# Performance work log

Measured on AMD Instinct MI355X. Metric: run time of the kernel, lower is better.

## Reference

```python
import jax, jax.numpy as jnp
import numpy as np

N, DIN, DH, DOUT, E, K = 8192, 1024, 4096, 1024, 8, 2
AUX_EPS = 1e-10


def setup_inputs() -> dict:
    key = jax.random.key(0)
    kx, kgw, kgb, kw1, kb1, kw2, kb2 = jax.random.split(key, 7)
    def init(k, shape, fan_in):
        return (jax.random.normal(k, shape, jnp.float32) / np.sqrt(fan_in)).astype(jnp.float32)
    return {
        "x": jax.random.normal(kx, (N, DIN), jnp.float32),
        "gate_w": init(kgw, (DIN, E), DIN),
        "gate_b": jnp.zeros((E,), jnp.float32),
        "w1": init(kw1, (E, DIN, DH), DIN),
        "b1": jnp.zeros((E, DH), jnp.float32),
        "w2": init(kw2, (E, DH, DOUT), DH),
        "b2": jnp.zeros((E, DOUT), jnp.float32),
    }


def reference(x, gate_w, gate_b, w1, b1, w2, b2):
    # Gating
    logits = x @ gate_w + gate_b                      # [N, E]
    probs = jax.nn.softmax(logits, axis=-1)           # [N, E]
    topk_vals, topk_idx = jax.lax.top_k(probs, K)     # [N, K]
    topk_norm = topk_vals / (topk_vals.sum(-1, keepdims=True) + AUX_EPS)

    # Scatter normalized top-k weights into a dense [N, E] combine matrix.
    n = x.shape[0]
    weights = jnp.zeros((n, E), x.dtype).at[jnp.arange(n)[:, None], topk_idx].add(topk_norm)

    # Dense all-expert FFN (same math: non-selected experts get weight 0).
    h = jax.nn.relu(jnp.einsum('nd,edh->neh', x, w1) + b1)   # [N, E, DH]
    y = jnp.einsum('neh,eho->neo', h, w2) + b2               # [N, E, DOUT]
    output = jnp.einsum('neo,ne->no', y, weights)            # [N, DOUT]

    # Aux load-balancing loss: KL(mean_probs || uniform)
    mean_probs = probs.mean(axis=0)
    aux_loss = jnp.sum(mean_probs * jnp.log(mean_probs * E + AUX_EPS))

    return output, aux_loss, probs
```

## Files before the change

### kernel.cpp

```cpp
#include <hip/hip_runtime.h>

#define NTOK 8192
#define DIN 1024
#define DH   4096
#define DOUT 1024
#define NE   8
#define MAXTILES 136
#define SLOTCAP  (MAXTILES*128)

typedef __bf16 bf16x8 __attribute__((ext_vector_type(8)));
typedef float  f32x4  __attribute__((ext_vector_type(4)));

constexpr size_t OFF_W1T  = 0;
constexpr size_t OFF_W2T  = 67108864;
constexpr size_t OFF_XB   = 134217728;
constexpr size_t OFF_H    = 150994944;
constexpr size_t OFF_SROW = 293601280;
constexpr size_t OFF_SW   = 293670912;
constexpr size_t OFF_TIDX = 293740544;
constexpr size_t OFF_TW   = 293806080;
constexpr size_t OFF_CTRL = 293871616;
constexpr size_t OFF_PART = 293871744;

__device__ __forceinline__ ushort f2bf(float f){
  unsigned u = __float_as_uint(f);
  u += 0x7fff + ((u >> 16) & 1);
  return (ushort)(u >> 16);
}

#define GLDS(g,l) __builtin_amdgcn_global_load_lds( \
    (const __attribute__((address_space(1))) void*)(g), \
    (__attribute__((address_space(3))) void*)(l), 16, 0, 0)

__global__ void k_cvt_x(const float4* __restrict__ x, ushort4* __restrict__ xb){
  int i = blockIdx.x * 256 + threadIdx.x;
  float4 v = x[i];
  ushort4 o;
  o.x = f2bf(v.x); o.y = f2bf(v.y); o.z = f2bf(v.z); o.w = f2bf(v.w);
  xb[i] = o;
}

__global__ void k_transpose(const float* __restrict__ W, ushort* __restrict__ WT, int R, int C){
  __shared__ ushort tl[64][72];
  int e  = blockIdx.z;
  int r0 = blockIdx.x * 64, c0 = blockIdx.y * 64;
  const float* Wp  = W  + (size_t)e * R * C;
  ushort*      WTp = WT + (size_t)e * R * C;
  int t = threadIdx.x;
  int lr  = t >> 4;
  int lc4 = t & 15;
#pragma unroll
  for (int i = 0; i < 4; i++){
    int r = lr + i * 16;
    float4 v = *(const float4*)(Wp + (size_t)(r0 + r) * C + c0 + lc4 * 4);
    ushort4 o; o.x = f2bf(v.x); o.y = f2bf(v.y); o.z = f2bf(v.z); o.w = f2bf(v.w);
    *(ushort4*)&tl[r][lc4 * 4] = o;
  }
  __syncthreads();
  int tr4 = t & 15;
  int tcc = t >> 4;
#pragma unroll
  for (int i = 0; i < 4; i++){
    int c = tcc + i * 16;
    ushort4 o;
    o.x = tl[tr4 * 4 + 0][c]; o.y = tl[tr4 * 4 + 1][c];
    o.z = tl[tr4 * 4 + 2][c]; o.w = tl[tr4 * 4 + 3][c];
    *(ushort4*)(WTp + (size_t)(c0 + c) * R + r0 + tr4 * 4) = o;
  }
}

__global__ void k_gate(const float* __restrict__ x, const float* __restrict__ gw,
                       const float* __restrict__ gb, float* __restrict__ probs_out,
                       int* __restrict__ topk_idx, float* __restrict__ topk_w,
                       int* __restrict__ count, float* __restrict__ partial){
  __shared__ float psum[8];
  __shared__ int   pcnt[8];
  int wv = threadIdx.x >> 6, lane = threadIdx.x & 63;
  int row = blockIdx.x * 4 + wv;
  if (threadIdx.x < 8){ psum[threadIdx.x] = 0.f; pcnt[threadIdx.x] = 0; }
  __syncthreads();

  const float4* x4 = (const float4*)(x + (size_t)row * DIN);
  float acc[8];
#pragma unroll
  for (int e = 0; e < 8; e++) acc[e] = 0.f;
#pragma unroll
  for (int j = 0; j < 4; j++){
    float4 v = x4[j * 64 + lane];
    int kbase = (j * 64 + lane) * 4;
#pragma unroll
    for (int c = 0; c < 4; c++){
      float xv = (&v.x)[c];
      const float4* g4 = (const float4*)(gw + (size_t)(kbase + c) * 8);
      float4 g0 = g4[0], g1 = g4[1];
      acc[0] += xv * g0.x; acc[1] += xv * g0.y; acc[2] += xv * g0.z; acc[3] += xv * g0.w;
      acc[4] += xv * g1.x; acc[5] += xv * g1.y; acc[6] += xv * g1.z; acc[7] += xv * g1.w;
    }
  }
#pragma unroll
  for (int e = 0; e < 8; e++)
#pragma unroll
    for (int off = 32; off; off >>= 1) acc[e] += __shfl_xor(acc[e], off, 64);

  float lg[8], p[8], mx = -1e30f, s = 0.f;
#pragma unroll
  for (int e = 0; e < 8; e++){ lg[e] = acc[e] + gb[e]; mx = fmaxf(mx, lg[e]); }
#pragma unroll
  for (int e = 0; e < 8; e++){ p[e] = expf(lg[e] - mx); s += p[e]; }
  float inv = 1.f / s;
#pragma unroll
  for (int e = 0; e < 8; e++) p[e] *= inv;

  if (lane < 8) probs_out[(size_t)row * 8 + lane] = p[lane];

  if (lane == 0){
    int i1 = 0; float v1 = p[0];
#pragma unroll
    for (int e = 1; e < 8; e++) if (p[e] > v1){ v1 = p[e]; i1 = e; }
    int i2 = -1; float v2 = -1.f;
#pragma unroll
    for (int e = 0; e < 8; e++){ if (e == i1) continue; if (p[e] > v2){ v2 = p[e]; i2 = e; } }
    float denom = 1.f / (v1 + v2 + 1e-10f);
    topk_idx[row * 2]     = i1;  topk_idx[row * 2 + 1] = i2;
    topk_w  [row * 2]     = v1 * denom;  topk_w[row * 2 + 1] = v2 * denom;
    atomicAdd(&pcnt[i1], 1); atomicAdd(&pcnt[i2], 1);
  }
  if (lane < 8) atomicAdd(&psum[lane], p[lane]);
  __syncthreads();
  if (threadIdx.x < 8){
    partial[(size_t)blockIdx.x * 8 + threadIdx.x] = psum[threadIdx.x];
    if (pcnt[threadIdx.x]) atomicAdd(&count[threadIdx.x], pcnt[threadIdx.x]);
  }
}

__global__ void k_aux(const float* __restrict__ partial, const int* __restrict__ count,
                      float* __restrict__ aux_out, int* __restrict__ tile_off){
  __shared__ float red[256];
  __shared__ float tot[8];
  int t = threadIdx.x, e = t & 7;
  float s = 0.f;
  for (int b = (t >> 3); b < 2048; b += 32) s += partial[(size_t)b * 8 + e];
  red[t] = s; __syncthreads();
  if (t < 8){ float v = 0.f; for (int c = 0; c < 32; c++) v += red[c * 8 + t]; tot[t] = v; }
  __syncthreads();
  if (t == 0){
    float aux = 0.f;
    for (int i = 0; i < 8; i++){
      float m = tot[i] * (1.f / 8192.f);
      aux += m * logf(m * 8.f + 1e-10f);
    }
    aux_out[0] = aux;
    int off = 0;
    for (int i = 0; i < 8; i++){ tile_off[i] = off; off += (count[i] + 127) >> 7; }
    tile_off[8] = off;
  }
}

__global__ void k_scatter(const int* __restrict__ topk_idx, const float* __restrict__ topk_w,
                          const int* __restrict__ tile_off, int* __restrict__ fill,
                          int* __restrict__ slot_row, float* __restrict__ slot_w){
  int i = blockIdx.x * 256 + threadIdx.x;
  int row = i >> 1;
  int e = topk_idx[i];
  float w = topk_w[i];
  int lane = threadIdx.x & 63;
  int pos = 0;
#pragma unroll
  for (int ex = 0; ex < 8; ex++){
    unsigned long long mask = __ballot(e == ex);
    if (e == ex){
      int leader = __ffsll((long long)mask) - 1;
      int base = 0;
      if (lane == leader) base = atomicAdd(&fill[ex], (int)__popcll(mask));
      base = __shfl(base, leader, 64);
      pos = base + (int)__popcll(mask & ((1ull << lane) - 1ull));
    }
  }
  int slot = tile_off[e] * 128 + pos;
  slot_row[slot] = row;
  slot_w[slot]   = w;
}


__global__ __launch_bounds__(256, 4) void k_gemm1(
    const ushort* __restrict__ xb, const ushort* __restrict__ w1t,
    const float* __restrict__ b1, const int* __restrict__ slot_row,
    const int* __restrict__ tile_off, ushort* __restrict__ H){
  __shared__ ushort As[128 * 64];
  __shared__ ushort Bs[128 * 64];
  int id = blockIdx.x;
  int pid = id >> 8, w = id & 255;
  int tileN = w & 31;
  int tileM = pid * 8 + (w >> 5);
  if (tileM >= tile_off[8]) return;
  int e = 0;
  while (e < 7 && tile_off[e + 1] <= tileM) e++;
  int m0 = tileM * 128, n0 = tileN * 128;
  int t = threadIdx.x;

  const ushort* aPtr[4]; const ushort* bPtr[4];
#pragma unroll
  for (int i = 0; i < 4; i++){
    int c = i * 256 + t, r = c >> 3, qp = c & 7;
    int q = qp ^ (r & 7);
    aPtr[i] = xb  + (size_t)slot_row[m0 + r] * DIN + q * 8;
    bPtr[i] = w1t + ((size_t)e * DH + n0 + r) * DIN + q * 8;
  }
  int wv = t >> 6, lane = t & 63;
  int wm = wv >> 1, wn = wv & 1, quad = lane >> 4, lc = lane & 15;
  f32x4 acc[4][4] = {};

  for (int k0 = 0; k0 < DIN; k0 += 64){
#pragma unroll
    for (int i = 0; i < 4; i++){
      int c = i * 256 + t;
      GLDS(aPtr[i] + k0, As + c * 8);
      GLDS(bPtr[i] + k0, Bs + c * 8);
    }
    __syncthreads();
#pragma unroll
    for (int kk = 0; kk < 2; kk++){
      bf16x8 a[4], b[4];
#pragma unroll
      for (int z = 0; z < 4; z++){
        int ra = wm * 64 + z * 16 + lc;
        a[z] = *(const bf16x8*)(As + ra * 64 + (((kk * 4 + quad) ^ (ra & 7)) * 8));
        int rb = wn * 64 + z * 16 + lc;
        b[z] = *(const bf16x8*)(Bs + rb * 64 + (((kk * 4 + quad) ^ (rb & 7)) * 8));
      }
#pragma unroll
      for (int zi = 0; zi < 4; zi++)
#pragma unroll
        for (int zj = 0; zj < 4; zj++)
          acc[zi][zj] = __builtin_amdgcn_mfma_f32_16x16x32_bf16(a[zi], b[zj], acc[zi][zj], 0, 0, 0);
    }
    __syncthreads();
  }

  const float* b1e = b1 + (size_t)e * DH;
#pragma unroll
  for (int i = 0; i < 4; i++){
#pragma unroll
    for (int r = 0; r < 4; r++){
      int slot = m0 + wm * 64 + i * 16 + quad * 4 + r;
      ushort* hrow = H + (size_t)slot * DH;
#pragma unroll
      for (int j = 0; j < 4; j++){
        int col = n0 + wn * 64 + j * 16 + lc;
        float v = acc[i][j][r] + b1e[col];
        hrow[col] = f2bf(fmaxf(v, 0.f));
      }
    }
  }
}

__global__ __launch_bounds__(256, 4) void k_gemm2(
    const ushort* __restrict__ H, const ushort* __restrict__ w2t,
    const float* __restrict__ b2, const int* __restrict__ slot_row,
    const float* __restrict__ slot_w, const int* __restrict__ tile_off,
    float* __restrict__ out){
  __shared__ ushort As[128 * 64];
  __shared__ ushort Bs[128 * 64];
  int id = blockIdx.x;
  int pid = id >> 7, w = id & 127;
  int tileN = w & 7;
  int tileM = pid * 16 + (w >> 3);
  if (tileM >= tile_off[8]) return;
  int e = 0;
  while (e < 7 && tile_off[e + 1] <= tileM) e++;
  int m0 = tileM * 128, n0 = tileN * 128;
  int t = threadIdx.x;

  const ushort* aPtr[4]; const ushort* bPtr[4];
#pragma unroll
  for (int i = 0; i < 4; i++){
    int c = i * 256 + t, r = c >> 3, qp = c & 7;
    int q = qp ^ (r & 7);
    aPtr[i] = H   + (size_t)(m0 + r) * DH + q * 8;
    bPtr[i] = w2t + ((size_t)e * DOUT + n0 + r) * DH + q * 8;
  }
  int wv = t >> 6, lane = t & 63;
  int wm = wv >> 1, wn = wv & 1, quad = lane >> 4, lc = lane & 15;
  f32x4 acc[4][4] = {};

  for (int k0 = 0; k0 < DH; k0 += 64){
#pragma unroll
    for (int i = 0; i < 4; i++){
      int c = i * 256 + t;
      GLDS(aPtr[i] + k0, As + c * 8);
      GLDS(bPtr[i] + k0, Bs + c * 8);
    }
    __syncthreads();
#pragma unroll
    for (int kk = 0; kk < 2; kk++){
      bf16x8 a[4], b[4];
#pragma unroll
      for (int z = 0; z < 4; z++){
        int ra = wm * 64 + z * 16 + lc;
        a[z] = *(const bf16x8*)(As + ra * 64 + (((kk * 4 + quad) ^ (ra & 7)) * 8));
        int rb = wn * 64 + z * 16 + lc;
        b[z] = *(const bf16x8*)(Bs + rb * 64 + (((kk * 4 + quad) ^ (rb & 7)) * 8));
      }
#pragma unroll
      for (int zi = 0; zi < 4; zi++)
#pragma unroll
        for (int zj = 0; zj < 4; zj++)
          acc[zi][zj] = __builtin_amdgcn_mfma_f32_16x16x32_bf16(a[zi], b[zj], acc[zi][zj], 0, 0, 0);
    }
    __syncthreads();
  }

  const float* b2e = b2 + (size_t)e * DOUT;
#pragma unroll
  for (int i = 0; i < 4; i++){
#pragma unroll
    for (int r = 0; r < 4; r++){
      int slot = m0 + wm * 64 + i * 16 + quad * 4 + r;
      float w2 = slot_w[slot];
      if (w2 == 0.f) continue;
      float* orow = out + (size_t)slot_row[slot] * DOUT;
#pragma unroll
      for (int j = 0; j < 4; j++){
        int col = n0 + wn * 64 + j * 16 + lc;
        atomicAdd(orow + col, w2 * (acc[i][j][r] + b2e[col]));
      }
    }
  }
}

extern "C" void kernel_launch(void* const* d_in, const int* in_sizes, int n_in,
                              void* d_out, int out_size, void* d_ws, size_t ws_size,
                              hipStream_t stream){
  const float* x      = (const float*)d_in[0];
  const float* gate_w = (const float*)d_in[1];
  const float* gate_b = (const float*)d_in[2];
  const float* w1     = (const float*)d_in[3];
  const float* b1     = (const float*)d_in[4];
  const float* w2     = (const float*)d_in[5];
  const float* b2     = (const float*)d_in[6];
  float* out = (float*)d_out;

  char* ws = (char*)d_ws;
  ushort* W1T   = (ushort*)(ws + OFF_W1T);
  ushort* W2T   = (ushort*)(ws + OFF_W2T);
  ushort* XB    = (ushort*)(ws + OFF_XB);
  ushort* H     = (ushort*)(ws + OFF_H);
  int*    SROW  = (int*)   (ws + OFF_SROW);
  float*  SW    = (float*) (ws + OFF_SW);
  int*    TIDX  = (int*)   (ws + OFF_TIDX);
  float*  TW    = (float*) (ws + OFF_TW);
  int*    COUNT = (int*)   (ws + OFF_CTRL);
  int*    FILL  = (int*)   (ws + OFF_CTRL + 32);
  int*    TOFF  = (int*)   (ws + OFF_CTRL + 64);
  float*  PART  = (float*) (ws + OFF_PART);

  float* aux_out   = out + (size_t)NTOK * DOUT;
  float* probs_out = aux_out + 1;

  hipMemsetAsync(d_out, 0, (size_t)out_size * 4, stream);
  hipMemsetAsync(ws + OFF_CTRL, 0, 128, stream);
  hipMemsetAsync(ws + OFF_SROW, 0, (size_t)SLOTCAP * 8, stream);

  k_cvt_x<<<dim3((NTOK * DIN / 4) / 256), 256, 0, stream>>>((const float4*)x, (ushort4*)XB);
  k_transpose<<<dim3(DIN / 64, DH / 64, NE), 256, 0, stream>>>(w1, W1T, DIN, DH);
  k_transpose<<<dim3(DH / 64, DOUT / 64, NE), 256, 0, stream>>>(w2, W2T, DH, DOUT);
  k_gate<<<dim3(NTOK / 4), 256, 0, stream>>>(x, gate_w, gate_b, probs_out, TIDX, TW, COUNT, PART);
  k_aux<<<dim3(1), 256, 0, stream>>>(PART, COUNT, aux_out, TOFF);
  k_scatter<<<dim3(NTOK * 2 / 256), 256, 0, stream>>>(TIDX, TW, TOFF, FILL, SROW, SW);
  k_gemm1<<<dim3(MAXTILES * (DH / 128)), 256, 0, stream>>>(XB, W1T, b1, SROW, TOFF, H);
  k_gemm2<<<dim3(MAXTILES * (DOUT / 128)), 256, 0, stream>>>(H, W2T, b2, SROW, SW, TOFF, out);
}
```

Measured before the change: 1.077 ms.

## Use 256x256 tiles with 32x32 MFMA and share one weight-transpose buffer

Both expert GEMMs move from 128x128 tiles with 256 threads and 16x16x32 MFMA to 256x256 tiles with 512 threads and 32x32x16 MFMA. Each wave now computes a 128x64 sub-tile, which raises arithmetic intensity per LDS read and per global load. Expert slots are padded to 256 rows instead of 128, which adds padding work, and the rows of an expert are no longer grouped across blocks. The w2 transpose now runs after gemm1 and reuses the w1 buffer, shrinking the workspace but serialising the transpose between the two GEMMs.

```diff
diff --git a/kernel.cpp b/kernel.cpp
--- a/kernel.cpp
+++ b/kernel.cpp
@@ -5,22 +5,21 @@
 #define DH   4096
 #define DOUT 1024
 #define NE   8
-#define MAXTILES 136
-#define SLOTCAP  (MAXTILES*128)
+#define MAXT256  72
+#define SLOTCAP  (MAXT256*256)
 
 typedef __bf16 bf16x8 __attribute__((ext_vector_type(8)));
-typedef float  f32x4  __attribute__((ext_vector_type(4)));
-
-constexpr size_t OFF_W1T  = 0;
-constexpr size_t OFF_W2T  = 67108864;
-constexpr size_t OFF_XB   = 134217728;
-constexpr size_t OFF_H    = 150994944;
-constexpr size_t OFF_SROW = 293601280;
-constexpr size_t OFF_SW   = 293670912;
-constexpr size_t OFF_TIDX = 293740544;
-constexpr size_t OFF_TW   = 293806080;
-constexpr size_t OFF_CTRL = 293871616;
-constexpr size_t OFF_PART = 293871744;
+typedef float  f32x16 __attribute__((ext_vector_type(16)));
+
+constexpr size_t OFF_WT   = 0;
+constexpr size_t OFF_XB   = 67108864;
+constexpr size_t OFF_SROW = 83886080;
+constexpr size_t OFF_SW   = 83959808;
+constexpr size_t OFF_TIDX = 84033536;
+constexpr size_t OFF_TW   = 84099072;
+constexpr size_t OFF_CTRL = 84164608;
+constexpr size_t OFF_PART = 84164736;
+constexpr size_t OFF_H    = 84230272;
 
 __device__ __forceinline__ ushort f2bf(float f){
   unsigned u = __float_as_uint(f);
@@ -151,7 +150,7 @@
     }
     aux_out[0] = aux;
     int off = 0;
-    for (int i = 0; i < 8; i++){ tile_off[i] = off; off += (count[i] + 127) >> 7; }
+    for (int i = 0; i < 8; i++){ tile_off[i] = off; off += (count[i] + 255) >> 8; }
     tile_off[8] = off;
   }
 }
@@ -176,153 +175,157 @@
       pos = base + (int)__popcll(mask & ((1ull << lane) - 1ull));
     }
   }
-  int slot = tile_off[e] * 128 + pos;
+  int slot = tile_off[e] * 256 + pos;
   slot_row[slot] = row;
   slot_w[slot]   = w;
 }
 
 
-__global__ __launch_bounds__(256, 4) void k_gemm1(
+__global__ __launch_bounds__(512, 2) void k_gemm1(
     const ushort* __restrict__ xb, const ushort* __restrict__ w1t,
     const float* __restrict__ b1, const int* __restrict__ slot_row,
     const int* __restrict__ tile_off, ushort* __restrict__ H){
-  __shared__ ushort As[128 * 64];
-  __shared__ ushort Bs[128 * 64];
+  __shared__ ushort As[256 * 64];
+  __shared__ ushort Bs[256 * 64];
   int id = blockIdx.x;
-  int pid = id >> 8, w = id & 255;
-  int tileN = w & 31;
-  int tileM = pid * 8 + (w >> 5);
+  int tileN = id & 15, tileM = id >> 4;
   if (tileM >= tile_off[8]) return;
   int e = 0;
   while (e < 7 && tile_off[e + 1] <= tileM) e++;
-  int m0 = tileM * 128, n0 = tileN * 128;
+  int m0 = tileM * 256, n0 = tileN * 256;
   int t = threadIdx.x;
 
-  const ushort* aPtr[4]; const ushort* bPtr[4];
+  const ushort* aP[4]; const ushort* bP[4];
 #pragma unroll
   for (int i = 0; i < 4; i++){
-    int c = i * 256 + t, r = c >> 3, qp = c & 7;
-    int q = qp ^ (r & 7);
-    aPtr[i] = xb  + (size_t)slot_row[m0 + r] * DIN + q * 8;
-    bPtr[i] = w1t + ((size_t)e * DH + n0 + r) * DIN + q * 8;
+    int c = i * 512 + t, r = c >> 3, q = (c & 7) ^ (r & 7);
+    aP[i] = xb  + (size_t)slot_row[m0 + r] * DIN + q * 8;
+    bP[i] = w1t + ((size_t)e * DH + n0 + r) * DIN + q * 8;
   }
   int wv = t >> 6, lane = t & 63;
-  int wm = wv >> 1, wn = wv & 1, quad = lane >> 4, lc = lane & 15;
-  f32x4 acc[4][4] = {};
+  int wm = wv >> 2, wn = wv & 3;
+  int lr = lane & 31, lk = lane >> 5;
+  f32x16 acc[4][2] = {};
 
   for (int k0 = 0; k0 < DIN; k0 += 64){
 #pragma unroll
     for (int i = 0; i < 4; i++){
-      int c = i * 256 + t;
-      GLDS(aPtr[i] + k0, As + c * 8);
-      GLDS(bPtr[i] + k0, Bs + c * 8);
+      int c = i * 512 + t;
+      GLDS(aP[i] + k0, As + c * 8);
+      GLDS(bP[i] + k0, Bs + c * 8);
     }
     __syncthreads();
 #pragma unroll
-    for (int kk = 0; kk < 2; kk++){
-      bf16x8 a[4], b[4];
-#pragma unroll
-      for (int z = 0; z < 4; z++){
-        int ra = wm * 64 + z * 16 + lc;
-        a[z] = *(const bf16x8*)(As + ra * 64 + (((kk * 4 + quad) ^ (ra & 7)) * 8));
-        int rb = wn * 64 + z * 16 + lc;
-        b[z] = *(const bf16x8*)(Bs + rb * 64 + (((kk * 4 + quad) ^ (rb & 7)) * 8));
-      }
-#pragma unroll
-      for (int zi = 0; zi < 4; zi++)
-#pragma unroll
-        for (int zj = 0; zj < 4; zj++)
-          acc[zi][zj] = __builtin_amdgcn_mfma_f32_16x16x32_bf16(a[zi], b[zj], acc[zi][zj], 0, 0, 0);
+    for (int kk = 0; kk < 4; kk++){
+      bf16x8 a[4], b[2];
+#pragma unroll
+      for (int mi = 0; mi < 4; mi++){
+        int r = wm * 128 + mi * 32 + lr;
+        a[mi] = *(const bf16x8*)(As + r * 64 + (((kk * 2 + lk) ^ (r & 7)) * 8));
+      }
+#pragma unroll
+      for (int nj = 0; nj < 2; nj++){
+        int r = wn * 64 + nj * 32 + lr;
+        b[nj] = *(const bf16x8*)(Bs + r * 64 + (((kk * 2 + lk) ^ (r & 7)) * 8));
+      }
+#pragma unroll
+      for (int mi = 0; mi < 4; mi++)
+#pragma unroll
+        for (int nj = 0; nj < 2; nj++)
+          acc[mi][nj] = __builtin_amdgcn_mfma_f32_32x32x16_bf16(a[mi], b[nj], acc[mi][nj], 0, 0, 0);
     }
     __syncthreads();
   }
 
   const float* b1e = b1 + (size_t)e * DH;
 #pragma unroll
-  for (int i = 0; i < 4; i++){
-#pragma unroll
-    for (int r = 0; r < 4; r++){
-      int slot = m0 + wm * 64 + i * 16 + quad * 4 + r;
-      ushort* hrow = H + (size_t)slot * DH;
-#pragma unroll
-      for (int j = 0; j < 4; j++){
-        int col = n0 + wn * 64 + j * 16 + lc;
-        float v = acc[i][j][r] + b1e[col];
-        hrow[col] = f2bf(fmaxf(v, 0.f));
-      }
-    }
-  }
-}
-
-__global__ __launch_bounds__(256, 4) void k_gemm2(
+  for (int mi = 0; mi < 4; mi++){
+#pragma unroll
+    for (int nj = 0; nj < 2; nj++){
+      int col = n0 + wn * 64 + nj * 32 + lr;
+      float bias = b1e[col];
+#pragma unroll
+      for (int reg = 0; reg < 16; reg++){
+        int row = (reg & 3) + 8 * (reg >> 2) + 4 * lk;
+        int slot = m0 + wm * 128 + mi * 32 + row;
+        float v = acc[mi][nj][reg] + bias;
+        H[(size_t)slot * DH + col] = f2bf(fmaxf(v, 0.f));
+      }
+    }
+  }
+}
+
+__global__ __launch_bounds__(512, 2) void k_gemm2(
     const ushort* __restrict__ H, const ushort* __restrict__ w2t,
     const float* __restrict__ b2, const int* __restrict__ slot_row,
     const float* __restrict__ slot_w, const int* __restrict__ tile_off,
     float* __restrict__ out){
-  __shared__ ushort As[128 * 64];
-  __shared__ ushort Bs[128 * 64];
+  __shared__ ushort As[256 * 64];
+  __shared__ ushort Bs[256 * 64];
   int id = blockIdx.x;
-  int pid = id >> 7, w = id & 127;
-  int tileN = w & 7;
-  int tileM = pid * 16 + (w >> 3);
+  int tileN = id & 3, tileM = id >> 2;
   if (tileM >= tile_off[8]) return;
   int e = 0;
   while (e < 7 && tile_off[e + 1] <= tileM) e++;
-  int m0 = tileM * 128, n0 = tileN * 128;
+  int m0 = tileM * 256, n0 = tileN * 256;
   int t = threadIdx.x;
 
-  const ushort* aPtr[4]; const ushort* bPtr[4];
+  const ushort* aP[4]; const ushort* bP[4];
 #pragma unroll
   for (int i = 0; i < 4; i++){
-    int c = i * 256 + t, r = c >> 3, qp = c & 7;
-    int q = qp ^ (r & 7);
-    aPtr[i] = H   + (size_t)(m0 + r) * DH + q * 8;
-    bPtr[i] = w2t + ((size_t)e * DOUT + n0 + r) * DH + q * 8;
+    int c = i * 512 + t, r = c >> 3, q = (c & 7) ^ (r & 7);
+    aP[i] = H   + (size_t)(m0 + r) * DH + q * 8;
+    bP[i] = w2t + ((size_t)e * DOUT + n0 + r) * DH + q * 8;
   }
   int wv = t >> 6, lane = t & 63;
-  int wm = wv >> 1, wn = wv & 1, quad = lane >> 4, lc = lane & 15;
-  f32x4 acc[4][4] = {};
+  int wm = wv >> 2, wn = wv & 3;
+  int lr = lane & 31, lk = lane >> 5;
+  f32x16 acc[4][2] = {};
 
   for (int k0 = 0; k0 < DH; k0 += 64){
 #pragma unroll
     for (int i = 0; i < 4; i++){
-      int c = i * 256 + t;
-      GLDS(aPtr[i] + k0, As + c * 8);
-      GLDS(bPtr[i] + k0, Bs + c * 8);
+      int c = i * 512 + t;
+      GLDS(aP[i] + k0, As + c * 8);
+      GLDS(bP[i] + k0, Bs + c * 8);
     }
     __syncthreads();
 #pragma unroll
-    for (int kk = 0; kk < 2; kk++){
-      bf16x8 a[4], b[4];
-#pragma unroll
-      for (int z = 0; z < 4; z++){
-        int ra = wm * 64 + z * 16 + lc;
-        a[z] = *(const bf16x8*)(As + ra * 64 + (((kk * 4 + quad) ^ (ra & 7)) * 8));
-        int rb = wn * 64 + z * 16 + lc;
-        b[z] = *(const bf16x8*)(Bs + rb * 64 + (((kk * 4 + quad) ^ (rb & 7)) * 8));
-      }
-#pragma unroll
-      for (int zi = 0; zi < 4; zi++)
-#pragma unroll
-        for (int zj = 0; zj < 4; zj++)
-          acc[zi][zj] = __builtin_amdgcn_mfma_f32_16x16x32_bf16(a[zi], b[zj], acc[zi][zj], 0, 0, 0);
+    for (int kk = 0; kk < 4; kk++){
+      bf16x8 a[4], b[2];
+#pragma unroll
+      for (int mi = 0; mi < 4; mi++){
+        int r = wm * 128 + mi * 32 + lr;
+        a[mi] = *(const bf16x8*)(As + r * 64 + (((kk * 2 + lk) ^ (r & 7)) * 8));
+      }
+#pragma unroll
+      for (int nj = 0; nj < 2; nj++){
+        int r = wn * 64 + nj * 32 + lr;
+        b[nj] = *(const bf16x8*)(Bs + r * 64 + (((kk * 2 + lk) ^ (r & 7)) * 8));
+      }
+#pragma unroll
+      for (int mi = 0; mi < 4; mi++)
+#pragma unroll
+        for (int nj = 0; nj < 2; nj++)
+          acc[mi][nj] = __builtin_amdgcn_mfma_f32_32x32x16_bf16(a[mi], b[nj], acc[mi][nj], 0, 0, 0);
     }
     __syncthreads();
   }
 
   const float* b2e = b2 + (size_t)e * DOUT;
 #pragma unroll
-  for (int i = 0; i < 4; i++){
-#pragma unroll
-    for (int r = 0; r < 4; r++){
-      int slot = m0 + wm * 64 + i * 16 + quad * 4 + r;
-      float w2 = slot_w[slot];
-      if (w2 == 0.f) continue;
+  for (int mi = 0; mi < 4; mi++){
+#pragma unroll
+    for (int reg = 0; reg < 16; reg++){
+      int row = (reg & 3) + 8 * (reg >> 2) + 4 * lk;
+      int slot = m0 + wm * 128 + mi * 32 + row;
+      float w = slot_w[slot];
+      if (w == 0.f) continue;
       float* orow = out + (size_t)slot_row[slot] * DOUT;
 #pragma unroll
-      for (int j = 0; j < 4; j++){
-        int col = n0 + wn * 64 + j * 16 + lc;
-        atomicAdd(orow + col, w2 * (acc[i][j][r] + b2e[col]));
+      for (int nj = 0; nj < 2; nj++){
+        int col = n0 + wn * 64 + nj * 32 + lr;
+        atomicAdd(orow + col, w * (acc[mi][nj][reg] + b2e[col]));
       }
     }
   }
@@ -341,8 +344,7 @@
   float* out = (float*)d_out;
 
   char* ws = (char*)d_ws;
-  ushort* W1T   = (ushort*)(ws + OFF_W1T);
-  ushort* W2T   = (ushort*)(ws + OFF_W2T);
+  ushort* WT    = (ushort*)(ws + OFF_WT);
   ushort* XB    = (ushort*)(ws + OFF_XB);
   ushort* H     = (ushort*)(ws + OFF_H);
   int*    SROW  = (int*)   (ws + OFF_SROW);
@@ -362,11 +364,11 @@
   hipMemsetAsync(ws + OFF_SROW, 0, (size_t)SLOTCAP * 8, stream);
 
   k_cvt_x<<<dim3((NTOK * DIN / 4) / 256), 256, 0, stream>>>((const float4*)x, (ushort4*)XB);
-  k_transpose<<<dim3(DIN / 64, DH / 64, NE), 256, 0, stream>>>(w1, W1T, DIN, DH);
-  k_transpose<<<dim3(DH / 64, DOUT / 64, NE), 256, 0, stream>>>(w2, W2T, DH, DOUT);
+  k_transpose<<<dim3(DIN / 64, DH / 64, NE), 256, 0, stream>>>(w1, WT, DIN, DH);
   k_gate<<<dim3(NTOK / 4), 256, 0, stream>>>(x, gate_w, gate_b, probs_out, TIDX, TW, COUNT, PART);
   k_aux<<<dim3(1), 256, 0, stream>>>(PART, COUNT, aux_out, TOFF);
   k_scatter<<<dim3(NTOK * 2 / 256), 256, 0, stream>>>(TIDX, TW, TOFF, FILL, SROW, SW);
-  k_gemm1<<<dim3(MAXTILES * (DH / 128)), 256, 0, stream>>>(XB, W1T, b1, SROW, TOFF, H);
-  k_gemm2<<<dim3(MAXTILES * (DOUT / 128)), 256, 0, stream>>>(H, W2T, b2, SROW, SW, TOFF, out);
-}
+  k_gemm1<<<dim3(MAXT256 * (DH / 256)), 512, 0, stream>>>(XB, WT, b1, SROW, TOFF, H);
+  k_transpose<<<dim3(DH / 64, DOUT / 64, NE), 256, 0, stream>>>(w2, WT, DH, DOUT);
+  k_gemm2<<<dim3(MAXT256 * (DOUT / 256)), 512, 0, stream>>>(H, WT, b2, SROW, SW, TOFF, out);
+}
```

Result: faster. 1.048 ms (-2.7%).

## Split hidden dimension into two chunks to keep H buffer cache-resident

Applied to the files above, without the earlier changes.

The hidden dimension is processed in two chunks of 2048. For each chunk, gemm1 writes a half-size H buffer and gemm2 consumes it, accumulating partial outputs atomically, with the bias added only on the first chunk. The intent is to shrink the H intermediate (about 70MB down to 35MB) so it can stay in the large last-level cache between the two GEMMs instead of round-tripping through HBM. The tile-to-block mapping also changes from a grouped 1D ordering to a plain 2D grid. The cost is twice as many atomic adds on the output, extra launches, and a smaller gemm1 grid per chunk.

```diff
diff --git a/kernel.cpp b/kernel.cpp
--- a/kernel.cpp
+++ b/kernel.cpp
@@ -5,6 +5,7 @@
 #define DH   4096
 #define DOUT 1024
 #define NE   8
+#define KC   2048
 #define MAXTILES 136
 #define SLOTCAP  (MAXTILES*128)
 
@@ -15,12 +16,12 @@
 constexpr size_t OFF_W2T  = 67108864;
 constexpr size_t OFF_XB   = 134217728;
 constexpr size_t OFF_H    = 150994944;
-constexpr size_t OFF_SROW = 293601280;
-constexpr size_t OFF_SW   = 293670912;
-constexpr size_t OFF_TIDX = 293740544;
-constexpr size_t OFF_TW   = 293806080;
-constexpr size_t OFF_CTRL = 293871616;
-constexpr size_t OFF_PART = 293871744;
+constexpr size_t OFF_SROW = 222298112;
+constexpr size_t OFF_SW   = 222367744;
+constexpr size_t OFF_TIDX = 222437376;
+constexpr size_t OFF_TW   = 222502912;
+constexpr size_t OFF_CTRL = 222568448;
+constexpr size_t OFF_PART = 222568576;
 
 __device__ __forceinline__ ushort f2bf(float f){
   unsigned u = __float_as_uint(f);
@@ -185,26 +186,22 @@
 __global__ __launch_bounds__(256, 4) void k_gemm1(
     const ushort* __restrict__ xb, const ushort* __restrict__ w1t,
     const float* __restrict__ b1, const int* __restrict__ slot_row,
-    const int* __restrict__ tile_off, ushort* __restrict__ H){
+    const int* __restrict__ tile_off, ushort* __restrict__ H, int dh0){
   __shared__ ushort As[128 * 64];
   __shared__ ushort Bs[128 * 64];
-  int id = blockIdx.x;
-  int pid = id >> 8, w = id & 255;
-  int tileN = w & 31;
-  int tileM = pid * 8 + (w >> 5);
+  int tileN = blockIdx.x, tileM = blockIdx.y;
   if (tileM >= tile_off[8]) return;
   int e = 0;
   while (e < 7 && tile_off[e + 1] <= tileM) e++;
   int m0 = tileM * 128, n0 = tileN * 128;
   int t = threadIdx.x;
 
-  const ushort* aPtr[4]; const ushort* bPtr[4];
-#pragma unroll
-  for (int i = 0; i < 4; i++){
-    int c = i * 256 + t, r = c >> 3, qp = c & 7;
-    int q = qp ^ (r & 7);
-    aPtr[i] = xb  + (size_t)slot_row[m0 + r] * DIN + q * 8;
-    bPtr[i] = w1t + ((size_t)e * DH + n0 + r) * DIN + q * 8;
+  const ushort* aP[4]; const ushort* bP[4];
+#pragma unroll
+  for (int i = 0; i < 4; i++){
+    int c = i * 256 + t, r = c >> 3, q = (c & 7) ^ (r & 7);
+    aP[i] = xb  + (size_t)slot_row[m0 + r] * DIN + q * 8;
+    bP[i] = w1t + ((size_t)e * DH + dh0 + n0 + r) * DIN + q * 8;
   }
   int wv = t >> 6, lane = t & 63;
   int wm = wv >> 1, wn = wv & 1, quad = lane >> 4, lc = lane & 15;
@@ -214,8 +211,8 @@
 #pragma unroll
     for (int i = 0; i < 4; i++){
       int c = i * 256 + t;
-      GLDS(aPtr[i] + k0, As + c * 8);
-      GLDS(bPtr[i] + k0, Bs + c * 8);
+      GLDS(aP[i] + k0, As + c * 8);
+      GLDS(bP[i] + k0, Bs + c * 8);
     }
     __syncthreads();
 #pragma unroll
@@ -237,13 +234,13 @@
     __syncthreads();
   }
 
-  const float* b1e = b1 + (size_t)e * DH;
+  const float* b1e = b1 + (size_t)e * DH + dh0;
 #pragma unroll
   for (int i = 0; i < 4; i++){
 #pragma unroll
     for (int r = 0; r < 4; r++){
       int slot = m0 + wm * 64 + i * 16 + quad * 4 + r;
-      ushort* hrow = H + (size_t)slot * DH;
+      ushort* hrow = H + (size_t)slot * KC;
 #pragma unroll
       for (int j = 0; j < 4; j++){
         int col = n0 + wn * 64 + j * 16 + lc;
@@ -258,37 +255,33 @@
     const ushort* __restrict__ H, const ushort* __restrict__ w2t,
     const float* __restrict__ b2, const int* __restrict__ slot_row,
     const float* __restrict__ slot_w, const int* __restrict__ tile_off,
-    float* __restrict__ out){
+    float* __restrict__ out, int dh0, int add_bias){
   __shared__ ushort As[128 * 64];
   __shared__ ushort Bs[128 * 64];
-  int id = blockIdx.x;
-  int pid = id >> 7, w = id & 127;
-  int tileN = w & 7;
-  int tileM = pid * 16 + (w >> 3);
+  int tileN = blockIdx.x, tileM = blockIdx.y;
   if (tileM >= tile_off[8]) return;
   int e = 0;
   while (e < 7 && tile_off[e + 1] <= tileM) e++;
   int m0 = tileM * 128, n0 = tileN * 128;
   int t = threadIdx.x;
 
-  const ushort* aPtr[4]; const ushort* bPtr[4];
-#pragma unroll
-  for (int i = 0; i < 4; i++){
-    int c = i * 256 + t, r = c >> 3, qp = c & 7;
-    int q = qp ^ (r & 7);
-    aPtr[i] = H   + (size_t)(m0 + r) * DH + q * 8;
-    bPtr[i] = w2t + ((size_t)e * DOUT + n0 + r) * DH + q * 8;
+  const ushort* aP[4]; const ushort* bP[4];
+#pragma unroll
+  for (int i = 0; i < 4; i++){
+    int c = i * 256 + t, r = c >> 3, q = (c & 7) ^ (r & 7);
+    aP[i] = H   + (size_t)(m0 + r) * KC + q * 8;
+    bP[i] = w2t + ((size_t)e * DOUT + n0 + r) * DH + dh0 + q * 8;
   }
   int wv = t >> 6, lane = t & 63;
   int wm = wv >> 1, wn = wv & 1, quad = lane >> 4, lc = lane & 15;
   f32x4 acc[4][4] = {};
 
-  for (int k0 = 0; k0 < DH; k0 += 64){
+  for (int k0 = 0; k0 < KC; k0 += 64){
 #pragma unroll
     for (int i = 0; i < 4; i++){
       int c = i * 256 + t;
-      GLDS(aPtr[i] + k0, As + c * 8);
-      GLDS(bPtr[i] + k0, Bs + c * 8);
+      GLDS(aP[i] + k0, As + c * 8);
+      GLDS(bP[i] + k0, Bs + c * 8);
     }
     __syncthreads();
 #pragma unroll
@@ -316,13 +309,14 @@
 #pragma unroll
     for (int r = 0; r < 4; r++){
       int slot = m0 + wm * 64 + i * 16 + quad * 4 + r;
-      float w2 = slot_w[slot];
-      if (w2 == 0.f) continue;
+      float w = slot_w[slot];
+      if (w == 0.f) continue;
       float* orow = out + (size_t)slot_row[slot] * DOUT;
 #pragma unroll
       for (int j = 0; j < 4; j++){
         int col = n0 + wn * 64 + j * 16 + lc;
-        atomicAdd(orow + col, w2 * (acc[i][j][r] + b2e[col]));
+        float bias = add_bias ? b2e[col] : 0.f;
+        atomicAdd(orow + col, w * (acc[i][j][r] + bias));
       }
     }
   }
@@ -367,6 +361,10 @@
   k_gate<<<dim3(NTOK / 4), 256, 0, stream>>>(x, gate_w, gate_b, probs_out, TIDX, TW, COUNT, PART);
   k_aux<<<dim3(1), 256, 0, stream>>>(PART, COUNT, aux_out, TOFF);
   k_scatter<<<dim3(NTOK * 2 / 256), 256, 0, stream>>>(TIDX, TW, TOFF, FILL, SROW, SW);
-  k_gemm1<<<dim3(MAXTILES * (DH / 128)), 256, 0, stream>>>(XB, W1T, b1, SROW, TOFF, H);
-  k_gemm2<<<dim3(MAXTILES * (DOUT / 128)), 256, 0, stream>>>(H, W2T, b2, SROW, SW, TOFF, out);
-}
+
+  for (int c = 0; c < DH / KC; c++){
+    int dh0 = c * KC;
+    k_gemm1<<<dim3(KC / 128, MAXTILES), 256, 0, stream>>>(XB, W1T, b1, SROW, TOFF, H, dh0);
+    k_gemm2<<<dim3(DOUT / 128, MAXTILES), 256, 0, stream>>>(H, W2T, b2, SROW, SW, TOFF, out, dh0, c == 0);
+  }
+}
```

New measurement: 1.199 ms. 1.11x slower.
